# Performance work log

Measured on AMD Instinct MI355X. Metric: run time of the kernel, lower is better.

The kernel has to match this reference:

```python
import jax, jax.numpy as jnp
import numpy as np

BETA_NORM = 1
ETA_THRESHOLD = 0.3
EPS = 1e-8


def setup_inputs() -> dict:
    key = jax.random.key(0)
    x = jax.random.normal(key, (4, 4096, 64), dtype=jnp.float32)
    return {"x": x}


def reference(x) -> jnp.ndarray:
    # x: (B, S, N) CSI input
    x_mag = jnp.abs(x)
    if BETA_NORM == 1:
        norms = jnp.sum(x_mag, axis=-1)                    # (B, S) L1 norm
    else:
        norms = jnp.sqrt(jnp.sum(x_mag * x_mag, axis=-1))  # (B, S) L2 norm

    B, S = norms.shape
    t = jnp.arange(S)[:, None]          # (S, 1)
    tau = jnp.arange(1, S)[None, :]     # (1, S-1) candidate lags
    j = t - tau                          # (S, S-1) index t - tau
    valid = j >= 0                       # tau <= t (triangular range)
    jc = jnp.clip(j, 0, S - 1)

    # norms[b, t - tau] gathered for all (t, tau): (B, S, S-1)
    past = norms[:, jc]
    eta_t = 1.0 - past / (norms[:, :, None] + EPS)
    crossed = valid[None, :, :] & (eta_t > ETA_THRESHOLD)

    # first (smallest) tau that crosses the threshold; 0 if none
    BIG = S  # sentinel larger than any valid tau
    tau_or_big = jnp.where(crossed, tau[None, :, :], BIG)  # (B, S, S-1)
    min_tau = jnp.min(tau_or_big, axis=-1)                 # (B, S)
    tc = jnp.where(min_tau < BIG, min_tau, 0).astype(jnp.float32)
    return tc
```

## Files before the change

kernel.cpp:

```cpp
#include <hip/hip_runtime.h>


#define DD 64
#define SS 4096

template <typename T>
__global__ void __launch_bounds__(256)
tc_norms_cmin_kernel(const float4* __restrict__ x4,
                     T* __restrict__ norms, T* __restrict__ cmin) {
    __shared__ T sn[64];
    int ci   = blockIdx.x;
    int wave = threadIdx.x >> 6;
    int lane = threadIdx.x & 63;
    int r0   = ci * 64 + wave * 16;

    #pragma unroll
    for (int k = 0; k < 4; ++k) {
        int rowbase = r0 + k * 4;
        float4 p = x4[rowbase * 16 + lane];
        T a = (T)fabsf(p.x) + (T)fabsf(p.y) + (T)fabsf(p.z) + (T)fabsf(p.w);
        #pragma unroll
        for (int off = 8; off > 0; off >>= 1)
            a += __shfl_xor(a, off, 64);
        if ((lane & 15) == 0) {
            int r = rowbase + (lane >> 4);
            norms[r] = a;
            sn[r - ci * 64] = a;
        }
    }
    __syncthreads();
    if (threadIdx.x < 64) {
        T m = sn[threadIdx.x];
        #pragma unroll
        for (int off = 32; off > 0; off >>= 1) {
            T o = __shfl_xor(m, off, 64);
            m = (o < m) ? o : m;
        }
        if (threadIdx.x == 0) cmin[ci] = m;
    }
}

template <typename T>
__global__ void __launch_bounds__(256)
tc_scan_kernel(const T* __restrict__ norms, const T* __restrict__ cmin,
               float* __restrict__ out) {
    int wave = threadIdx.x >> 6;
    int lane = threadIdx.x & 63;
    int gw   = blockIdx.x * 4 + wave;
    int t0   = gw * 4;
    int b    = t0 >> 12;
    int tr0  = t0 & (SS - 1);
    int c    = tr0 >> 6;
    const T* row = norms + (b << 12);

    T v  = row[(c << 6) + lane];
    T cm = cmin[(b << 6) + lane];

    int cached_cc = -1;
    T v2 = (T)0;
    float res[4];
    #pragma unroll
    for (int k = 0; k < 4; ++k) {
        int tr  = tr0 + k;
        int pos = tr & 63;
        T thr = (T)0.7 * (__shfl(v, pos, 64) + (T)1e-8);
        int r = 0;
        unsigned long long m = __ballot(lane < pos && v < thr);
        if (m) {
            r = tr - ((c << 6) + (63 - __clzll(m)));
        } else {
            unsigned long long mc = __ballot(lane < c && cm < thr);
            if (mc) {
                int cc = 63 - __clzll(mc);
                if (cc != cached_cc) {
                    v2 = row[(cc << 6) + lane];
                    cached_cc = cc;
                }
                unsigned long long m2 = __ballot(v2 < thr);
                r = tr - ((cc << 6) + (63 - __clzll(m2)));
            }
        }
        res[k] = (float)r;
    }
    if (lane == 0) {
        float4 o = make_float4(res[0], res[1], res[2], res[3]);
        ((float4*)out)[gw] = o;
    }
}

extern "C" void kernel_launch(void* const* d_in, const int* in_sizes, int n_in,
                              void* d_out, int out_size, void* d_ws, size_t ws_size,
                              hipStream_t stream) {
    const float* x = (const float*)d_in[0];
    float* out = (float*)d_out;
    int total  = in_sizes[0];
    int nrows  = total / DD;
    int nchunk = nrows / 64;

    int grdA = nchunk;
    int grdB = nrows / 16;

    if (ws_size >= (size_t)(nrows + nchunk) * sizeof(double)) {
        double* nrm = (double*)d_ws;
        double* cmn = nrm + nrows;
        tc_norms_cmin_kernel<double><<<grdA, 256, 0, stream>>>((const float4*)x, nrm, cmn);
        tc_scan_kernel<double><<<grdB, 256, 0, stream>>>(nrm, cmn, out);
    } else {
        float* nrm = (float*)d_ws;
        float* cmn = nrm + nrows;
        tc_norms_cmin_kernel<float><<<grdA, 256, 0, stream>>>((const float4*)x, nrm, cmn);
        tc_scan_kernel<float><<<grdB, 256, 0, stream>>>(nrm, cmn, out);
    }
}
```

Before: 58.11 us.

## Fuse norm and scan kernels into one cooperative kernel with grid sync

Replaces the two-kernel pipeline (norms/chunk-min, then scan) with a single cooperative launch that computes norms, does a grid-wide sync, then scans using the block's shared-memory norms. It removes one kernel launch and reuses the norms held in shared memory instead of reloading them. The cost is a grid.sync barrier across 256 blocks and the cooperative launch path. The old two-kernel path is kept as a fallback if the cooperative launch fails, and it drops the float fallback when workspace is small.

```diff
diff --git a/kernel.cpp b/kernel.cpp
--- a/kernel.cpp
+++ b/kernel.cpp
@@ -1,8 +1,84 @@
 #include <hip/hip_runtime.h>
+#include <hip/hip_cooperative_groups.h>
+
+namespace cg = cooperative_groups;
 
 
 #define DD 64
 #define SS 4096
+
+__global__ void __launch_bounds__(256)
+tc_fused_kernel(const float4* __restrict__ x4, double* __restrict__ nrm,
+                double* __restrict__ cmn, float* __restrict__ out) {
+    cg::grid_group grid = cg::this_grid();
+    __shared__ double sn[64];
+
+    int ci   = blockIdx.x;
+    int wave = threadIdx.x >> 6;
+    int lane = threadIdx.x & 63;
+
+    int r0 = ci * 64 + wave * 16;
+    #pragma unroll
+    for (int k = 0; k < 4; ++k) {
+        int rowbase = r0 + k * 4;
+        float4 p = x4[rowbase * 16 + lane];
+        double a = (double)fabsf(p.x) + (double)fabsf(p.y) +
+                   (double)fabsf(p.z) + (double)fabsf(p.w);
+        #pragma unroll
+        for (int off = 8; off > 0; off >>= 1)
+            a += __shfl_xor(a, off, 64);
+        if ((lane & 15) == 0) {
+            int r = rowbase + (lane >> 4);
+            nrm[r] = a;
+            sn[r - ci * 64] = a;
+        }
+    }
+    __syncthreads();
+    if (threadIdx.x < 64) {
+        double m = sn[threadIdx.x];
+        #pragma unroll
+        for (int off = 32; off > 0; off >>= 1) {
+            double o = __shfl_xor(m, off, 64);
+            m = (o < m) ? o : m;
+        }
+        if (threadIdx.x == 0) cmn[ci] = m;
+    }
+    __threadfence();
+    grid.sync();
+
+    int b = ci >> 6;
+    int c = ci & 63;
+    double v  = sn[lane];
+    double cm = cmn[(b << 6) + lane];
+
+    int cached_cc = -1;
+    double v2 = 0.0;
+    float myres = 0.0f;
+    #pragma unroll 4
+    for (int k = 0; k < 16; ++k) {
+        int pos = wave * 16 + k;
+        double thr = 0.7 * (sn[pos] + 1e-8);
+        int r = 0;
+        unsigned long long m = __ballot(lane < pos && v < thr);
+        if (m) {
+            r = pos - (63 - __clzll(m));
+        } else {
+            unsigned long long mc = __ballot(lane < c && cm < thr);
+            if (mc) {
+                int cc = 63 - __clzll(mc);
+                if (cc != cached_cc) {
+                    v2 = nrm[(b << 12) + (cc << 6) + lane];
+                    cached_cc = cc;
+                }
+                unsigned long long m2 = __ballot(v2 < thr);
+                r = ((c - cc) << 6) + pos - (63 - __clzll(m2));
+            }
+        }
+        if (lane == k) myres = (float)r;
+    }
+    if (lane < 16)
+        out[(b << 12) + (c << 6) + wave * 16 + lane] = myres;
+}
 
 template <typename T>
 __global__ void __launch_bounds__(256)
@@ -13,7 +89,6 @@
     int wave = threadIdx.x >> 6;
     int lane = threadIdx.x & 63;
     int r0   = ci * 64 + wave * 16;
-
     #pragma unroll
     for (int k = 0; k < 4; ++k) {
         int rowbase = r0 + k * 4;
@@ -91,24 +166,21 @@
 extern "C" void kernel_launch(void* const* d_in, const int* in_sizes, int n_in,
                               void* d_out, int out_size, void* d_ws, size_t ws_size,
                               hipStream_t stream) {
-    const float* x = (const float*)d_in[0];
+    const float4* x4 = (const float4*)d_in[0];
     float* out = (float*)d_out;
     int total  = in_sizes[0];
     int nrows  = total / DD;
     int nchunk = nrows / 64;
 
-    int grdA = nchunk;
-    int grdB = nrows / 16;
+    double* nrm = (double*)d_ws;
+    double* cmn = nrm + nrows;
 
-    if (ws_size >= (size_t)(nrows + nchunk) * sizeof(double)) {
-        double* nrm = (double*)d_ws;
-        double* cmn = nrm + nrows;
-        tc_norms_cmin_kernel<double><<<grdA, 256, 0, stream>>>((const float4*)x, nrm, cmn);
-        tc_scan_kernel<double><<<grdB, 256, 0, stream>>>(nrm, cmn, out);
-    } else {
-        float* nrm = (float*)d_ws;
-        float* cmn = nrm + nrows;
-        tc_norms_cmin_kernel<float><<<grdA, 256, 0, stream>>>((const float4*)x, nrm, cmn);
-        tc_scan_kernel<float><<<grdB, 256, 0, stream>>>(nrm, cmn, out);
+    void* args[] = { (void*)&x4, (void*)&nrm, (void*)&cmn, (void*)&out };
+    hipError_t rc = hipLaunchCooperativeKernel(
+        (const void*)tc_fused_kernel, dim3(nchunk), dim3(256), args, 0, stream);
+
+    if (rc != hipSuccess) {
+        tc_norms_cmin_kernel<double><<<nchunk, 256, 0, stream>>>(x4, nrm, cmn);
+        tc_scan_kernel<double><<<nrows / 16, 256, 0, stream>>>(nrm, cmn, out);
     }
 }
```

New measurement: 103.0 us. 1.77x slower.

## Fuse norm and scan kernels with cross-block chunk-min signaling

Applied to the files above, without the earlier changes.

Merges the norm/chunk-min kernel and the scan kernel into one launch. Each block of 1024 threads computes the norms of its 64-row chunk, publishes the chunk minimum with a release atomic store, then spin-waits on acquire loads for the minima of earlier chunks. After a bounded spin it falls back to recomputing missing chunk norms straight from x. This removes the second launch and the global round trip for the chunk's own norms, at the cost of inter-block busy-waiting. The workspace is never cleared, so stale positive values left from a previous call would be accepted as ready, and the float fallback for a small workspace is gone.

```diff
diff --git a/kernel.cpp b/kernel.cpp
--- a/kernel.cpp
+++ b/kernel.cpp
@@ -1,114 +1,144 @@
 #include <hip/hip_runtime.h>
 
 
-#define DD 64
 #define SS 4096
+typedef unsigned long long u64;
 
-template <typename T>
-__global__ void __launch_bounds__(256)
-tc_norms_cmin_kernel(const float4* __restrict__ x4,
-                     T* __restrict__ norms, T* __restrict__ cmin) {
-    __shared__ T sn[64];
-    int ci   = blockIdx.x;
-    int wave = threadIdx.x >> 6;
-    int lane = threadIdx.x & 63;
-    int r0   = ci * 64 + wave * 16;
-
-    #pragma unroll
-    for (int k = 0; k < 4; ++k) {
-        int rowbase = r0 + k * 4;
-        float4 p = x4[rowbase * 16 + lane];
-        T a = (T)fabsf(p.x) + (T)fabsf(p.y) + (T)fabsf(p.z) + (T)fabsf(p.w);
+__device__ __noinline__ double chunk_norms_from_x(
+    const float4* __restrict__ x4, int globalChunk, int lane,
+    volatile double* scratch)
+{
+    double mn = 1e300;
+    int g = lane >> 4;
+    int e = lane & 15;
+    for (int r = 0; r < 16; ++r) {
+        int row = globalChunk * 64 + r * 4 + g;
+        float4 p = x4[row * 16 + e];
+        double a = (double)fabsf(p.x) + (double)fabsf(p.y)
+                 + (double)fabsf(p.z) + (double)fabsf(p.w);
         #pragma unroll
         for (int off = 8; off > 0; off >>= 1)
             a += __shfl_xor(a, off, 64);
-        if ((lane & 15) == 0) {
-            int r = rowbase + (lane >> 4);
-            norms[r] = a;
-            sn[r - ci * 64] = a;
-        }
+        if (e == 0) scratch[r * 4 + g] = a;
+        mn = (a < mn) ? a : mn;
+    }
+    #pragma unroll
+    for (int off = 16; off < 64; off <<= 1) {
+        double o = __shfl_xor(mn, off, 64);
+        mn = (o < mn) ? o : mn;
+    }
+    return mn;
+}
+
+__global__ void __launch_bounds__(1024)
+tc_fused_kernel(const float4* __restrict__ x4, double* __restrict__ nrm,
+                double* __restrict__ cmn, float* __restrict__ out)
+{
+    __shared__ double sn[64];
+    __shared__ double sfall[16][64];
+
+    int ci   = blockIdx.x;
+    int b    = ci >> 6;
+    int c    = ci & 63;
+    int wave = threadIdx.x >> 6;
+    int lane = threadIdx.x & 63;
+    int g    = lane >> 4;
+    int e    = lane & 15;
+
+    {
+        int rlocal = wave * 4 + g;
+        int row    = ci * 64 + rlocal;
+        float4 p = x4[row * 16 + e];
+        double a = (double)fabsf(p.x) + (double)fabsf(p.y)
+                 + (double)fabsf(p.z) + (double)fabsf(p.w);
+        #pragma unroll
+        for (int off = 8; off > 0; off >>= 1)
+            a += __shfl_xor(a, off, 64);
+        if (e == 0) { nrm[row] = a; sn[rlocal] = a; }
     }
     __syncthreads();
     if (threadIdx.x < 64) {
-        T m = sn[threadIdx.x];
+        double m = sn[lane];
         #pragma unroll
         for (int off = 32; off > 0; off >>= 1) {
-            T o = __shfl_xor(m, off, 64);
+            double o = __shfl_xor(m, off, 64);
             m = (o < m) ? o : m;
         }
-        if (threadIdx.x == 0) cmin[ci] = m;
+        if (lane == 0) {
+            __threadfence();
+            __hip_atomic_store((u64*)&cmn[ci], __builtin_bit_cast(u64, m),
+                               __ATOMIC_RELEASE, __HIP_MEMORY_SCOPE_AGENT);
+        }
     }
-}
 
-template <typename T>
-__global__ void __launch_bounds__(256)
-tc_scan_kernel(const T* __restrict__ norms, const T* __restrict__ cmin,
-               float* __restrict__ out) {
-    int wave = threadIdx.x >> 6;
-    int lane = threadIdx.x & 63;
-    int gw   = blockIdx.x * 4 + wave;
-    int t0   = gw * 4;
-    int b    = t0 >> 12;
-    int tr0  = t0 & (SS - 1);
-    int c    = tr0 >> 6;
-    const T* row = norms + (b << 12);
+    const u64* cp = (const u64*)(cmn + (b << 6) + lane);
+    double cm = __builtin_bit_cast(double,
+        __hip_atomic_load(cp, __ATOMIC_ACQUIRE, __HIP_MEMORY_SCOPE_AGENT));
+    int spins = 0;
+    bool timeout = false;
+    while (__ballot((lane < c) && !(cm > 0.0))) {
+        if (++spins > (1 << 20)) { timeout = true; break; }
+        __builtin_amdgcn_s_sleep(8);
+        cm = __builtin_bit_cast(double,
+            __hip_atomic_load(cp, __ATOMIC_ACQUIRE, __HIP_MEMORY_SCOPE_AGENT));
+    }
+    u64 ready = ~0ull;
+    if (timeout) {
+        ready = __ballot(cm > 0.0);
+        for (int j = 0; j < c; ++j) {
+            if (!((ready >> j) & 1)) {
+                double m = chunk_norms_from_x(x4, (b << 6) + j, lane, sfall[wave]);
+                if (lane == j) cm = m;
+            }
+        }
+    }
 
-    T v  = row[(c << 6) + lane];
-    T cm = cmin[(b << 6) + lane];
-
+    double v = sn[lane];
     int cached_cc = -1;
-    T v2 = (T)0;
+    double v2 = 0.0;
     float res[4];
     #pragma unroll
     for (int k = 0; k < 4; ++k) {
-        int tr  = tr0 + k;
-        int pos = tr & 63;
-        T thr = (T)0.7 * (__shfl(v, pos, 64) + (T)1e-8);
+        int pos = wave * 4 + k;
+        double thr = 0.7 * (sn[pos] + 1e-8);
         int r = 0;
-        unsigned long long m = __ballot(lane < pos && v < thr);
+        u64 m = __ballot(lane < pos && v < thr);
         if (m) {
-            r = tr - ((c << 6) + (63 - __clzll(m)));
+            r = pos - (63 - __clzll(m));
         } else {
-            unsigned long long mc = __ballot(lane < c && cm < thr);
+            u64 mc = __ballot(lane < c && cm < thr);
             if (mc) {
                 int cc = 63 - __clzll(mc);
                 if (cc != cached_cc) {
-                    v2 = row[(cc << 6) + lane];
+                    if ((ready >> cc) & 1) {
+                        v2 = nrm[(b << 12) + (cc << 6) + lane];
+                    } else {
+                        chunk_norms_from_x(x4, (b << 6) + cc, lane, sfall[wave]);
+                        v2 = sfall[wave][lane];
+                    }
                     cached_cc = cc;
                 }
-                unsigned long long m2 = __ballot(v2 < thr);
-                r = tr - ((cc << 6) + (63 - __clzll(m2)));
+                u64 m2 = __ballot(v2 < thr);
+                r = ((c - cc) << 6) + pos - (63 - __clzll(m2));
             }
         }
         res[k] = (float)r;
     }
-    if (lane == 0) {
-        float4 o = make_float4(res[0], res[1], res[2], res[3]);
-        ((float4*)out)[gw] = o;
-    }
+    if (lane == 0)
+        ((float4*)out)[ci * 16 + wave] =
+            make_float4(res[0], res[1], res[2], res[3]);
 }
 
 extern "C" void kernel_launch(void* const* d_in, const int* in_sizes, int n_in,
                               void* d_out, int out_size, void* d_ws, size_t ws_size,
                               hipStream_t stream) {
-    const float* x = (const float*)d_in[0];
+    const float4* x4 = (const float4*)d_in[0];
     float* out = (float*)d_out;
-    int total  = in_sizes[0];
-    int nrows  = total / DD;
+    int nrows  = in_sizes[0] / 64;
     int nchunk = nrows / 64;
 
-    int grdA = nchunk;
-    int grdB = nrows / 16;
+    double* nrm = (double*)d_ws;
+    double* cmn = nrm + nrows;
 
-    if (ws_size >= (size_t)(nrows + nchunk) * sizeof(double)) {
-        double* nrm = (double*)d_ws;
-        double* cmn = nrm + nrows;
-        tc_norms_cmin_kernel<double><<<grdA, 256, 0, stream>>>((const float4*)x, nrm, cmn);
-        tc_scan_kernel<double><<<grdB, 256, 0, stream>>>(nrm, cmn, out);
-    } else {
-        float* nrm = (float*)d_ws;
-        float* cmn = nrm + nrows;
-        tc_norms_cmin_kernel<float><<<grdA, 256, 0, stream>>>((const float4*)x, nrm, cmn);
-        tc_scan_kernel<float><<<grdB, 256, 0, stream>>>(nrm, cmn, out);
-    }
+    tc_fused_kernel<<<nchunk, 1024, 0, stream>>>(x4, nrm, cmn, out);
 }
```

Result: slower. 146.2 us (+151.6%).
